# Performance work log

Measured on AMD Instinct MI355X. Metric: run time of the kernel, lower is better.

## Reference

```python
import jax, jax.numpy as jnp
import numpy as np

NEG_INF = -10000000.0


def setup_inputs() -> dict:
    key = jax.random.key(0)
    ks = jax.random.split(key, 9)
    B, S, H = 16, 2048, 1024
    std = 1.0 / np.sqrt(H)
    return {
        "queries": jax.random.normal(ks[0], (B, S, H), jnp.float32),
        "keys": jax.random.normal(ks[1], (B, S, H), jnp.float32),
        "values": jax.random.normal(ks[2], (B, S, H), jnp.float32),
        "Wq": jax.random.normal(ks[3], (H, H), jnp.float32) * std,
        "bq": jax.random.normal(ks[4], (H,), jnp.float32) * std,
        "Wk": jax.random.normal(ks[5], (H, H), jnp.float32) * std,
        "bk": jax.random.normal(ks[6], (H,), jnp.float32) * std,
        "Wv": jax.random.normal(ks[7], (H, H), jnp.float32) * std,
        "bv": jax.random.normal(ks[8], (H,), jnp.float32) * std,
    }


def reference(queries, keys, values, Wq, bq, Wk, bk, Wv, bv):
    H = queries.shape[-1]
    scale = jnp.asarray(1.0, queries.dtype) / jnp.sqrt(jnp.asarray(H, queries.dtype))
    # nn.Linear: x @ W.T + b
    q = queries @ Wq.T + bq          # [B, Q, H]
    k = keys @ Wk.T + bk             # [B, S, H]
    v = values @ Wv.T + bv           # [B, S, H]
    # torch: unnorm = k.bmm(q^T) -> [B, S, Q]; permuted to [B, Q, S] before softmax.
    scores = jnp.einsum('bqh,bsh->bqs', q, k) * scale   # [B, Q, S]
    Qlen, Slen = scores.shape[1], scores.shape[2]
    # tril(ones, diagonal=-1) on [S, Q]: entry (s, q) masked when s > q.
    # In the permuted [q, s] layout: mask where s > q (causal).
    mask = jnp.where(jnp.arange(Slen)[None, :] > jnp.arange(Qlen)[:, None],
                     jnp.asarray(NEG_INF, scores.dtype),
                     jnp.asarray(0.0, scores.dtype))
    attention_weights = jax.nn.softmax(scores + mask, axis=-1)  # [B, Q, S]
    context = jnp.einsum('bqs,bsh->bqh', attention_weights, v)  # [B, Q, H]
    # module returns attention_weights permuted back to [B, S, Q]
    return context, attention_weights.transpose(0, 2, 1)
```

## Files before the change

kernel.cpp:

```cpp
#include <hip/hip_runtime.h>
#include <hip/hip_bf16.h>
#include <cstdint>


typedef unsigned short u16;
typedef __bf16 bfrag __attribute__((ext_vector_type(8)));
typedef float f32x4 __attribute__((ext_vector_type(4)));

#define DEVI __device__ __forceinline__

DEVI u16 f2bf(float f) {
  unsigned u = __builtin_bit_cast(unsigned, f);
  u += 0x7FFFu + ((u >> 16) & 1u);
  return (u16)(u >> 16);
}

DEVI void g2l16(const void* g, void* l) {
  __builtin_amdgcn_global_load_lds(
      (const __attribute__((address_space(1))) void*)g,
      (__attribute__((address_space(3))) void*)l, 16, 0, 0);
}

__global__ void cast_f32_to_bf16(const float* __restrict__ in, u16* __restrict__ out, long n4) {
  long i = (long)blockIdx.x * blockDim.x + threadIdx.x;
  long stride = (long)gridDim.x * blockDim.x;
  for (long j = i; j < n4; j += stride) {
    float4 v = ((const float4*)in)[j];
    ushort4 o;
    o.x = f2bf(v.x); o.y = f2bf(v.y); o.z = f2bf(v.z); o.w = f2bf(v.w);
    ((ushort4*)out)[j] = o;
  }
}

template<int OUT_F32, int BIAS_MODE, int CAUSAL>
__global__ __launch_bounds__(512, 2)
void gemm_nt256(const u16* __restrict__ A, const u16* __restrict__ B,
                void* __restrict__ Cv, const float* __restrict__ bias,
                float scale, int K, long sA, long sB, long sC, int ldc,
                int gx, int gy)
{
  int nwg = gridDim.x * gridDim.y * gridDim.z;
  int hbid = blockIdx.x + gridDim.x * (blockIdx.y + gridDim.y * blockIdx.z);
  int cpx = nwg >> 3;
  int l = (hbid & 7) * cpx + (hbid >> 3);
  int bx = l % gx;
  int rest = l / gx;
  int by = rest % gy;
  int bz = rest / gy;
  if (CAUSAL == 2) by = (gy - 1) - by;

  long n0 = (long)bx * 256;
  long m0 = (long)by * 256;
  if (CAUSAL == 1 && m0 > n0 + 255) return;
  const u16* Ab = A + (long)bz * sA;
  const u16* Bb = B + (long)bz * sB;

  __shared__ __align__(16) u16 lA[2][256 * 64];
  __shared__ __align__(16) u16 lB[2][256 * 64];

  int tid = threadIdx.x;
  int lane = tid & 63;
  int wid = tid >> 6;
  int wr = wid >> 2;
  int wc = wid & 3;

  f32x4 acc[8][4] = {};

  int kmax = (CAUSAL == 2) ? ((K < m0 + 256) ? K : (int)(m0 + 256)) : K;
  int nkt = kmax >> 6;

  auto stage = [&](int kt, int bsel) {
    long k0 = (long)kt << 6;
    #pragma unroll
    for (int i = 0; i < 4; ++i) {
      int c = tid + (i << 9);
      int row = c >> 3;
      int sc = (c & 7) ^ (row & 7);
      g2l16(Ab + (m0 + row) * (long)K + k0 + (sc << 3), (char*)lA[bsel] + c * 16);
      g2l16(Bb + (n0 + row) * (long)K + k0 + (sc << 3), (char*)lB[bsel] + c * 16);
    }
  };

  stage(0, 0);
  __syncthreads();
  int cur = 0;
  for (int t = 0; t < nkt; ++t) {
    if (t + 1 < nkt) stage(t + 1, cur ^ 1);
    const char* la = (const char*)lA[cur];
    const char* lb = (const char*)lB[cur];
    #pragma unroll
    for (int k2 = 0; k2 < 2; ++k2) {
      int kbc = (k2 << 2) + (lane >> 4);
      int rsel = lane & 15;
      bfrag af[8], bf[4];
      #pragma unroll
      for (int f = 0; f < 8; ++f) {
        int ra = wr * 128 + f * 16 + rsel;
        af[f] = *(const bfrag*)(la + ra * 128 + ((kbc ^ (ra & 7)) << 4));
      }
      #pragma unroll
      for (int f = 0; f < 4; ++f) {
        int rb = wc * 64 + f * 16 + rsel;
        bf[f] = *(const bfrag*)(lb + rb * 128 + ((kbc ^ (rb & 7)) << 4));
      }
      #pragma unroll
      for (int mi = 0; mi < 8; ++mi)
        #pragma unroll
        for (int ni = 0; ni < 4; ++ni)
          acc[mi][ni] = __builtin_amdgcn_mfma_f32_16x16x32_bf16(af[mi], bf[ni], acc[mi][ni], 0, 0, 0);
    }
    __syncthreads();
    cur ^= 1;
  }

  long cmb = m0 + wr * 128 + (lane >> 4) * 4;
  long cnb = n0 + wc * 64 + (lane & 15);
  #pragma unroll
  for (int mi = 0; mi < 8; ++mi) {
    #pragma unroll
    for (int ni = 0; ni < 4; ++ni) {
      f32x4 v = acc[mi][ni];
      long col = cnb + ni * 16;
      #pragma unroll
      for (int i = 0; i < 4; ++i) {
        long row = cmb + mi * 16 + i;
        float x = v[i] * scale;
        if (BIAS_MODE == 1) x += bias[col];
        if (BIAS_MODE == 2) x += bias[row];
        long cidx = (long)bz * sC + row * ldc + col;
        if (OUT_F32) ((float*)Cv)[cidx] = x;
        else         ((u16*)Cv)[cidx] = f2bf(x);
      }
    }
  }
}

__global__ __launch_bounds__(512)
void softmax_stats(const float* __restrict__ att, float* __restrict__ mo,
                   float* __restrict__ lo, int S) {
  int b  = blockIdx.y;
  int q0 = blockIdx.x * 64;
  int t  = threadIdx.x;
  int ql = t & 63;
  int grp = t >> 6;
  int q = q0 + ql;
  const float* a = att + (long)b * S * S + q;
  int send = q0 + 64;
  float m = -3.0e38f, l = 0.0f;
  for (int s = grp; s < send; s += 8) {
    float v = (s <= q) ? a[(long)s * S] : -3.0e38f;
    float mn = fmaxf(m, v);
    l = l * __expf(m - mn) + __expf(v - mn);
    m = mn;
  }
  __shared__ float sm[8][64], sl[8][64];
  sm[grp][ql] = m;
  sl[grp][ql] = l;
  __syncthreads();
  if (t < 64) {
    float M = sm[0][t];
    #pragma unroll
    for (int g = 1; g < 8; ++g) M = fmaxf(M, sm[g][t]);
    float L = 0.0f;
    #pragma unroll
    for (int g = 0; g < 8; ++g) L += sl[g][t] * __expf(sm[g][t] - M);
    mo[(long)b * S + q0 + t] = M;
    lo[(long)b * S + q0 + t] = L;
  }
}

__global__ void norm_transpose(float* __restrict__ att, const float* __restrict__ ms,
                               const float* __restrict__ ls, u16* __restrict__ probs, int S) {
  int b  = blockIdx.z;
  int q0 = blockIdx.x * 64;
  int s0 = blockIdx.y * 64;
  float* a = att + (long)b * S * S;
  u16* p = probs + (long)b * S * S;
  int tid = threadIdx.x;
  bool needp = s0 < ((q0 & ~255) + 256);

  if (s0 > q0 + 63) {
    float4 z = make_float4(0.f, 0.f, 0.f, 0.f);
    ushort4 zu; zu.x = zu.y = zu.z = zu.w = 0;
    #pragma unroll
    for (int it = 0; it < 4; ++it) {
      int j = tid + it * 256; int row = j >> 4; int c4 = (j & 15) * 4;
      *(float4*)&a[(long)(s0 + row) * S + q0 + c4] = z;
      if (needp) *(ushort4*)&p[(long)(q0 + row) * S + s0 + c4] = zu;
    }
    return;
  }

  __shared__ float t[64][65];
  __shared__ float lm[64], lr[64];
  if (tid < 64) {
    lm[tid] = ms[(long)b * S + q0 + tid];
    lr[tid] = 1.0f / ls[(long)b * S + q0 + tid];
  }
  __syncthreads();

  #pragma unroll
  for (int it = 0; it < 4; ++it) {
    int j = tid + it * 256; int row = j >> 4; int c4 = (j & 15) * 4;
    int s = s0 + row;
    float4 v = *(const float4*)&a[(long)s * S + q0 + c4];
    float vv[4] = {v.x, v.y, v.z, v.w};
    float oo[4];
    #pragma unroll
    for (int e = 0; e < 4; ++e) {
      int q = q0 + c4 + e;
      float pv = (s <= q) ? __expf(vv[e] - lm[c4 + e]) * lr[c4 + e] : 0.0f;
      oo[e] = pv;
      t[row][c4 + e] = pv;
    }
    float4 ov; ov.x = oo[0]; ov.y = oo[1]; ov.z = oo[2]; ov.w = oo[3];
    *(float4*)&a[(long)s * S + q0 + c4] = ov;
  }
  __syncthreads();

  #pragma unroll
  for (int it = 0; it < 4; ++it) {
    int j = tid + it * 256; int qrow = j >> 4; int sc4 = (j & 15) * 4;
    ushort4 ov;
    ov.x = f2bf(t[sc4 + 0][qrow]);
    ov.y = f2bf(t[sc4 + 1][qrow]);
    ov.z = f2bf(t[sc4 + 2][qrow]);
    ov.w = f2bf(t[sc4 + 3][qrow]);
    *(ushort4*)&p[(long)(q0 + qrow) * S + s0 + sc4] = ov;
  }
}

extern "C" void kernel_launch(void* const* d_in, const int* in_sizes, int n_in,
                              void* d_out, int out_size, void* d_ws, size_t ws_size,
                              hipStream_t stream) {
  const int B = 16, S = 2048, H = 1024;
  const long NE = (long)B * S * H;
  const float* Q  = (const float*)d_in[0];
  const float* Kk = (const float*)d_in[1];
  const float* V  = (const float*)d_in[2];
  const float* Wq = (const float*)d_in[3];
  const float* bq = (const float*)d_in[4];
  const float* Wk = (const float*)d_in[5];
  const float* bk = (const float*)d_in[6];
  const float* Wv = (const float*)d_in[7];
  const float* bv = (const float*)d_in[8];

  char* ws = (char*)d_ws;
  u16* xq    = (u16*)ws;
  u16* xk    = (u16*)(ws + (64L << 20));
  u16* xv    = (u16*)(ws + (128L << 20));
  u16* qb    = (u16*)(ws + (192L << 20));
  u16* kb    = (u16*)ws;
  u16* vT    = (u16*)(ws + (64L << 20));
  u16* probs = (u16*)(ws + (128L << 20));
  u16* Wqb   = (u16*)(ws + (256L << 20));
  u16* Wkb   = (u16*)(ws + (256L << 20) + (2L << 20));
  u16* Wvb   = (u16*)(ws + (256L << 20) + (4L << 20));
  float* mbuf = (float*)(ws + (256L << 20) + (6L << 20));
  float* lbuf = (float*)(ws + (256L << 20) + (6L << 20) + (1L << 17));

  float* ctx = (float*)d_out;
  float* att = (float*)d_out + NE;

  cast_f32_to_bf16<<<2048, 256, 0, stream>>>(Q,  xq, NE >> 2);
  cast_f32_to_bf16<<<2048, 256, 0, stream>>>(Kk, xk, NE >> 2);
  cast_f32_to_bf16<<<2048, 256, 0, stream>>>(V,  xv, NE >> 2);
  cast_f32_to_bf16<<<512, 256, 0, stream>>>(Wq, Wqb, ((long)H * H) >> 2);
  cast_f32_to_bf16<<<512, 256, 0, stream>>>(Wk, Wkb, ((long)H * H) >> 2);
  cast_f32_to_bf16<<<512, 256, 0, stream>>>(Wv, Wvb, ((long)H * H) >> 2);

  gemm_nt256<0, 1, 0><<<dim3(4, 128, 1), 512, 0, stream>>>(
      xq, Wqb, qb, bq, 1.0f, H, 0, 0, 0, H, 4, 128);
  gemm_nt256<0, 1, 0><<<dim3(4, 128, 1), 512, 0, stream>>>(
      xk, Wkb, kb, bk, 1.0f, H, 0, 0, 0, H, 4, 128);
  gemm_nt256<0, 2, 0><<<dim3(8, 4, 16), 512, 0, stream>>>(
      Wvb, xv, vT, bv, 1.0f, H, 0, (long)S * H, (long)H * S, S, 8, 4);

  gemm_nt256<1, 0, 1><<<dim3(8, 8, 16), 512, 0, stream>>>(
      kb, qb, att, nullptr, 0.03125f, H, (long)S * H, (long)S * H,
      (long)S * S, S, 8, 8);

  softmax_stats<<<dim3(32, 16), 512, 0, stream>>>(att, mbuf, lbuf, S);

  norm_transpose<<<dim3(32, 32, 16), 256, 0, stream>>>(att, mbuf, lbuf, probs, S);

  gemm_nt256<1, 0, 2><<<dim3(4, 8, 16), 512, 0, stream>>>(
      probs, vT, ctx, nullptr, 1.0f, S, (long)S * S, (long)H * S,
      (long)S * H, H, 4, 8);
}
```

Measured before the change: 813.8 us.

## Fuse softmax max/sum partials into score GEMM epilogue and zero masked tiles there

The score GEMM now computes per-column partial softmax max and sum statistics from its accumulators and writes them to a small buffer. A tiny reduction kernel combines the partials, replacing the separate strided pass that reread the full score matrix. Fully masked 256x256 tiles are zeroed directly in the GEMM so norm_transpose can skip them. This cuts a large read of the fp32 score matrix, at the cost of extra epilogue work and one more block-wide sync.

```diff
diff --git a/kernel.cpp b/kernel.cpp
--- a/kernel.cpp
+++ b/kernel.cpp
@@ -32,10 +32,11 @@
   }
 }
 
-template<int OUT_F32, int BIAS_MODE, int CAUSAL>
+template<int OUT_F32, int BIAS_MODE, int CAUSAL, int STATS>
 __global__ __launch_bounds__(512, 2)
 void gemm_nt256(const u16* __restrict__ A, const u16* __restrict__ B,
                 void* __restrict__ Cv, const float* __restrict__ bias,
+                float* __restrict__ pm, float* __restrict__ pl,
                 float scale, int K, long sA, long sB, long sC, int ldc,
                 int gx, int gy)
 {
@@ -51,14 +52,27 @@
 
   long n0 = (long)bx * 256;
   long m0 = (long)by * 256;
-  if (CAUSAL == 1 && m0 > n0 + 255) return;
+  int tid = threadIdx.x;
+
+  if (CAUSAL == 1 && m0 > n0 + 255) {
+    float4 z = make_float4(0.f, 0.f, 0.f, 0.f);
+    float* C = (float*)Cv + (long)bz * sC;
+    #pragma unroll
+    for (int i = 0; i < 32; ++i) {
+      int e = tid + (i << 9);
+      int row = e >> 6;
+      int c4 = (e & 63) << 2;
+      *(float4*)&C[(m0 + row) * (long)ldc + n0 + c4] = z;
+    }
+    return;
+  }
+
   const u16* Ab = A + (long)bz * sA;
   const u16* Bb = B + (long)bz * sB;
 
   __shared__ __align__(16) u16 lA[2][256 * 64];
   __shared__ __align__(16) u16 lB[2][256 * 64];
 
-  int tid = threadIdx.x;
   int lane = tid & 63;
   int wid = tid >> 6;
   int wr = wid >> 2;
@@ -133,40 +147,74 @@
       }
     }
   }
-}
-
-__global__ __launch_bounds__(512)
-void softmax_stats(const float* __restrict__ att, float* __restrict__ mo,
-                   float* __restrict__ lo, int S) {
-  int b  = blockIdx.y;
-  int q0 = blockIdx.x * 64;
-  int t  = threadIdx.x;
-  int ql = t & 63;
-  int grp = t >> 6;
-  int q = q0 + ql;
-  const float* a = att + (long)b * S * S + q;
-  int send = q0 + 64;
-  float m = -3.0e38f, l = 0.0f;
-  for (int s = grp; s < send; s += 8) {
-    float v = (s <= q) ? a[(long)s * S] : -3.0e38f;
-    float mn = fmaxf(m, v);
-    l = l * __expf(m - mn) + __expf(v - mn);
-    m = mn;
-  }
-  __shared__ float sm[8][64], sl[8][64];
-  sm[grp][ql] = m;
-  sl[grp][ql] = l;
-  __syncthreads();
-  if (t < 64) {
-    float M = sm[0][t];
-    #pragma unroll
-    for (int g = 1; g < 8; ++g) M = fmaxf(M, sm[g][t]);
-    float L = 0.0f;
-    #pragma unroll
-    for (int g = 0; g < 8; ++g) L += sl[g][t] * __expf(sm[g][t] - M);
-    mo[(long)b * S + q0 + t] = M;
-    lo[(long)b * S + q0 + t] = L;
-  }
+
+  if (STATS) {
+    float* pml = (float*)&lA[0][0];
+    #pragma unroll
+    for (int ni = 0; ni < 4; ++ni) {
+      long col = cnb + ni * 16;
+      float m = -3.0e38f;
+      #pragma unroll
+      for (int mi = 0; mi < 8; ++mi)
+        #pragma unroll
+        for (int i = 0; i < 4; ++i) {
+          long row = cmb + mi * 16 + i;
+          float v = acc[mi][ni][i] * scale;
+          if (row <= col) m = fmaxf(m, v);
+        }
+      float lsum = 0.f;
+      #pragma unroll
+      for (int mi = 0; mi < 8; ++mi)
+        #pragma unroll
+        for (int i = 0; i < 4; ++i) {
+          long row = cmb + mi * 16 + i;
+          float v = acc[mi][ni][i] * scale;
+          lsum += (row <= col) ? __expf(v - m) : 0.f;
+        }
+      #pragma unroll
+      for (int w = 16; w <= 32; w <<= 1) {
+        float m2 = __shfl_xor(m, w);
+        float l2 = __shfl_xor(lsum, w);
+        float M = fmaxf(m, m2);
+        lsum = lsum * __expf(m - M) + l2 * __expf(m2 - M);
+        m = M;
+      }
+      if ((lane >> 4) == 0) {
+        int tcol = wc * 64 + ni * 16 + lane;
+        pml[wr * 256 + tcol] = m;
+        pml[512 + wr * 256 + tcol] = lsum;
+      }
+    }
+    __syncthreads();
+    if (tid < 256) {
+      float ma = pml[tid], mb2 = pml[256 + tid];
+      float la_ = pml[512 + tid], lb_ = pml[768 + tid];
+      float M = fmaxf(ma, mb2);
+      float L = la_ * __expf(ma - M) + lb_ * __expf(mb2 - M);
+      long st = m0 >> 8;
+      long qi = n0 + tid;
+      pm[((long)bz * 8 + st) * 2048 + qi] = M;
+      pl[((long)bz * 8 + st) * 2048 + qi] = L;
+    }
+  }
+}
+
+__global__ __launch_bounds__(256)
+void stats_reduce(const float* __restrict__ pm, const float* __restrict__ pl,
+                  float* __restrict__ mo, float* __restrict__ lo) {
+  int idx = blockIdx.x * 256 + threadIdx.x;
+  int b = idx >> 11, q = idx & 2047;
+  float M = -3.0e38f, L = 0.f;
+  int stmax = q >> 8;
+  for (int st = 0; st <= stmax; ++st) {
+    float m2 = pm[((long)b * 8 + st) * 2048 + q];
+    float l2 = pl[((long)b * 8 + st) * 2048 + q];
+    float Mn = fmaxf(M, m2);
+    L = L * __expf(M - Mn) + l2 * __expf(m2 - Mn);
+    M = Mn;
+  }
+  mo[(long)b * 2048 + q] = M;
+  lo[(long)b * 2048 + q] = L;
 }
 
 __global__ void norm_transpose(float* __restrict__ att, const float* __restrict__ ms,
@@ -180,12 +228,14 @@
   bool needp = s0 < ((q0 & ~255) + 256);
 
   if (s0 > q0 + 63) {
+    bool skipped256 = (s0 >> 8) > (q0 >> 8);
+    if (skipped256 && !needp) return;
     float4 z = make_float4(0.f, 0.f, 0.f, 0.f);
     ushort4 zu; zu.x = zu.y = zu.z = zu.w = 0;
     #pragma unroll
     for (int it = 0; it < 4; ++it) {
       int j = tid + it * 256; int row = j >> 4; int c4 = (j & 15) * 4;
-      *(float4*)&a[(long)(s0 + row) * S + q0 + c4] = z;
+      if (!skipped256) *(float4*)&a[(long)(s0 + row) * S + q0 + c4] = z;
       if (needp) *(ushort4*)&p[(long)(q0 + row) * S + s0 + c4] = zu;
     }
     return;
@@ -256,8 +306,10 @@
   u16* Wqb   = (u16*)(ws + (256L << 20));
   u16* Wkb   = (u16*)(ws + (256L << 20) + (2L << 20));
   u16* Wvb   = (u16*)(ws + (256L << 20) + (4L << 20));
-  float* mbuf = (float*)(ws + (256L << 20) + (6L << 20));
-  float* lbuf = (float*)(ws + (256L << 20) + (6L << 20) + (1L << 17));
+  float* mbuf = (float*)(ws + (262L << 20));
+  float* lbuf = (float*)(ws + (262L << 20) + (1L << 17));
+  float* pm   = (float*)(ws + (263L << 20));
+  float* pl   = (float*)(ws + (264L << 20));
 
   float* ctx = (float*)d_out;
   float* att = (float*)d_out + NE;
@@ -269,22 +321,23 @@
   cast_f32_to_bf16<<<512, 256, 0, stream>>>(Wk, Wkb, ((long)H * H) >> 2);
   cast_f32_to_bf16<<<512, 256, 0, stream>>>(Wv, Wvb, ((long)H * H) >> 2);
 
-  gemm_nt256<0, 1, 0><<<dim3(4, 128, 1), 512, 0, stream>>>(
-      xq, Wqb, qb, bq, 1.0f, H, 0, 0, 0, H, 4, 128);
-  gemm_nt256<0, 1, 0><<<dim3(4, 128, 1), 512, 0, stream>>>(
-      xk, Wkb, kb, bk, 1.0f, H, 0, 0, 0, H, 4, 128);
-  gemm_nt256<0, 2, 0><<<dim3(8, 4, 16), 512, 0, stream>>>(
-      Wvb, xv, vT, bv, 1.0f, H, 0, (long)S * H, (long)H * S, S, 8, 4);
-
-  gemm_nt256<1, 0, 1><<<dim3(8, 8, 16), 512, 0, stream>>>(
-      kb, qb, att, nullptr, 0.03125f, H, (long)S * H, (long)S * H,
+  gemm_nt256<0, 1, 0, 0><<<dim3(4, 128, 1), 512, 0, stream>>>(
+      xq, Wqb, qb, bq, nullptr, nullptr, 1.0f, H, 0, 0, 0, H, 4, 128);
+  gemm_nt256<0, 1, 0, 0><<<dim3(4, 128, 1), 512, 0, stream>>>(
+      xk, Wkb, kb, bk, nullptr, nullptr, 1.0f, H, 0, 0, 0, H, 4, 128);
+  gemm_nt256<0, 2, 0, 0><<<dim3(8, 4, 16), 512, 0, stream>>>(
+      Wvb, xv, vT, bv, nullptr, nullptr, 1.0f, H, 0, (long)S * H,
+      (long)H * S, S, 8, 4);
+
+  gemm_nt256<1, 0, 1, 1><<<dim3(8, 8, 16), 512, 0, stream>>>(
+      kb, qb, att, nullptr, pm, pl, 0.03125f, H, (long)S * H, (long)S * H,
       (long)S * S, S, 8, 8);
 
-  softmax_stats<<<dim3(32, 16), 512, 0, stream>>>(att, mbuf, lbuf, S);
+  stats_reduce<<<128, 256, 0, stream>>>(pm, pl, mbuf, lbuf);
 
   norm_transpose<<<dim3(32, 32, 16), 256, 0, stream>>>(att, mbuf, lbuf, probs, S);
 
-  gemm_nt256<1, 0, 2><<<dim3(4, 8, 16), 512, 0, stream>>>(
-      probs, vT, ctx, nullptr, 1.0f, S, (long)S * S, (long)H * S,
-      (long)S * H, H, 4, 8);
-}
+  gemm_nt256<1, 0, 2, 0><<<dim3(4, 8, 16), 512, 0, stream>>>(
+      probs, vT, ctx, nullptr, nullptr, nullptr, 1.0f, S, (long)S * S,
+      (long)H * S, (long)S * H, H, 4, 8);
+}
```

Result: faster. 730.3 us (median of 2 runs) (-10.3%).
